# Kernel tuning notes

Hardware: AMD Instinct MI355X
Metric: run time of the kernel (lower is better)

## Reference

```python
import jax, jax.numpy as jnp
import numpy as np

B, T, C, H = 512, 256, 512, 64  # batch, block_size, n_embedding, head_size


def setup_inputs() -> dict:
    key = jax.random.key(0)
    kx, kq, kk, kv = jax.random.split(key, 4)
    # nn.Linear(C, H, bias=False) default init ~ U(-1/sqrt(C), 1/sqrt(C)); stored as x @ W
    s = 1.0 / np.sqrt(C)
    return {
        "x": jax.random.normal(kx, (B, T, C), dtype=jnp.float32),
        "Wq": jax.random.uniform(kq, (C, H), jnp.float32, -s, s),
        "Wk": jax.random.uniform(kk, (C, H), jnp.float32, -s, s),
        "Wv": jax.random.uniform(kv, (C, H), jnp.float32, -s, s),
    }


def reference(x, Wq, Wk, Wv):
    # Projections (bias=False Linear)
    q = x @ Wq  # [B,T,H]
    k = x @ Wk  # [B,T,H]
    v = x @ Wv  # [B,T,H]
    scale = k.shape[-1] ** -0.5
    wei = jnp.einsum('bqh,bkh->bqk', q, k) * scale  # [B,T,T]
    causal = jnp.tril(jnp.ones((x.shape[1], x.shape[1]), dtype=bool))
    wei = jnp.where(causal, wei, -jnp.inf)
    wei = jax.nn.softmax(wei, axis=-1)
    # dropout p=0.0 (eval-mode reference) -> identity
    return wei @ v  # [B,T,H]
```

## Files before the change

kernel.cpp:

```cpp
#include <hip/hip_runtime.h>
#include <hip/hip_bf16.h>

typedef __bf16 bf16;
typedef __bf16 bf16x8 __attribute__((ext_vector_type(8)));
typedef __bf16 bf16x4 __attribute__((ext_vector_type(4)));
typedef float  f32x4  __attribute__((ext_vector_type(4)));

#define MFMA16(a,b,c) __builtin_amdgcn_mfma_f32_16x16x32_bf16((a),(b),(c),0,0,0)

__device__ __forceinline__ void gld16(const void* g, void* l) {
    __builtin_amdgcn_global_load_lds(
        (const __attribute__((address_space(1))) void*)g,
        (__attribute__((address_space(3))) void*)l, 16, 0, 0);
}


__global__ void __launch_bounds__(256) wt_frag_kernel(
        const float* __restrict__ Wq, const float* __restrict__ Wk,
        const float* __restrict__ Wv, bf16* __restrict__ WTfrag) {
    int tid = blockIdx.x * 256 + threadIdx.x;
    int j  = tid & 7;
    int l  = (tid >> 3) & 63;
    int f  = tid >> 9;
    int nf = f % 12;
    int KC = f / 12;
    int k   = KC * 32 + (l >> 4) * 8 + j;
    int col = (nf & 3) * 16 + (l & 15);
    const float* W = (nf < 4) ? Wq : ((nf < 8) ? Wk : Wv);
    WTfrag[tid] = (bf16)W[k * 64 + col];
}

__global__ void __launch_bounds__(256, 1) fused_kernel(
        const float* __restrict__ x, const bf16* __restrict__ WTfrag,
        float* __restrict__ out) {
    extern __shared__ char smem[];

    const int tid = threadIdx.x;
    const int l   = tid & 63;
    const int w   = tid >> 6;
    const int lo  = l & 15;
    const int hi  = l >> 4;
    const int b   = blockIdx.x;
    const char* xb = (const char*)x + (size_t)b * 524288;
    const char* wb = (const char*)WTfrag;

    auto stage = [&](int buf, int kc) {
        #pragma unroll
        for (int j = 0; j < 8; ++j) {
            const int s   = j * 256 + tid;
            const int row = s >> 3;
            const int uP  = s & 7;
            const int uL  = uP ^ (row & 7);
            gld16(xb + (size_t)row * 2048 + kc * 128 + uL * 16,
                  smem + buf * 32768 + s * 16);
        }
        #pragma unroll
        for (int j = 0; j < 3; ++j) {
            const int s = j * 256 + tid;
            gld16(wb + kc * 12288 + s * 16,
                  smem + 65536 + buf * 12288 + s * 16);
        }
    };

    f32x4 acc[4][12];
    #pragma unroll
    for (int mq = 0; mq < 4; ++mq)
        #pragma unroll
        for (int nf = 0; nf < 12; ++nf)
            acc[mq][nf] = (f32x4){0.f, 0.f, 0.f, 0.f};

    auto compute = [&](int buf) {
        bf16x8 a[4];
        #pragma unroll
        for (int mq = 0; mq < 4; ++mq) {
            const int row = w * 64 + mq * 16 + lo;
            const int u0  = (hi * 2)     ^ (lo & 7);
            const int u1  = (hi * 2 + 1) ^ (lo & 7);
            f32x4 v0 = *(const f32x4*)(smem + buf * 32768 + row * 128 + u0 * 16);
            f32x4 v1 = *(const f32x4*)(smem + buf * 32768 + row * 128 + u1 * 16);
            bf16x8 t;
            t[0] = (bf16)v0[0]; t[1] = (bf16)v0[1]; t[2] = (bf16)v0[2]; t[3] = (bf16)v0[3];
            t[4] = (bf16)v1[0]; t[5] = (bf16)v1[1]; t[6] = (bf16)v1[2]; t[7] = (bf16)v1[3];
            a[mq] = t;
        }
        #pragma unroll
        for (int nf = 0; nf < 12; ++nf) {
            bf16x8 bf_ = *(const bf16x8*)(smem + 65536 + buf * 12288 +
                                          nf * 1024 + l * 16);
            #pragma unroll
            for (int mq = 0; mq < 4; ++mq)
                acc[mq][nf] = MFMA16(a[mq], bf_, acc[mq][nf]);
        }
    };

    stage(0, 0);

    #pragma unroll 1
    for (int k = 0; k < 16; ++k) {
        __builtin_amdgcn_s_barrier();
        if (k + 1 < 16) {
            stage((k + 1) & 1, k + 1);
            asm volatile("s_waitcnt vmcnt(11)" ::: "memory");
        } else {
            asm volatile("s_waitcnt vmcnt(0)" ::: "memory");
        }
        __builtin_amdgcn_s_barrier();
        __builtin_amdgcn_sched_barrier(0);
        compute(k & 1);
    }

    __syncthreads();
    {
        char* Qb = smem;
        char* Kb = smem + 32768;
        char* Vb = smem + 65536;
        #pragma unroll
        for (int nf = 0; nf < 12; ++nf) {
            #pragma unroll
            for (int mq = 0; mq < 4; ++mq) {
                #pragma unroll
                for (int i = 0; i < 4; ++i) {
                    bf16 v = (bf16)acc[mq][nf][i];
                    if (nf < 8) {
                        const int row = w * 64 + mq * 16 + hi * 4 + i;
                        const int col = (nf & 3) * 16 + lo;
                        const int u   = col >> 3;
                        char* base = (nf < 4) ? Qb : Kb;
                        *(bf16*)(base + row * 128 + ((u ^ (row & 7)) << 4) +
                                 (col & 7) * 2) = v;
                    } else {
                        const int h = (nf - 8) * 16 + lo;
                        const int t = w * 64 + mq * 16 + hi * 4 + i;
                        const int u = t >> 3;
                        *(bf16*)(Vb + h * 512 + ((u ^ (h & 7)) << 4) +
                                 (t & 7) * 2) = v;
                    }
                }
            }
        }
    }
    __syncthreads();

    const char* Qb = smem;
    const char* Kb = smem + 32768;
    const char* Vb = smem + 65536;
    bf16* Pl = (bf16*)(smem + 98304) + w * (16 * 72);

    bf16x8 qfr[4][2];
    #pragma unroll
    for (int qf = 0; qf < 4; ++qf)
        #pragma unroll
        for (int ks = 0; ks < 2; ++ks) {
            const int q = qf * 64 + w * 16 + lo;
            const int u = ks * 4 + hi;
            qfr[qf][ks] = *(const bf16x8*)(Qb + q * 128 + ((u ^ (lo & 7)) << 4));
        }

    f32x4 o[4][4];
    #pragma unroll
    for (int qf = 0; qf < 4; ++qf)
        #pragma unroll
        for (int mf = 0; mf < 4; ++mf)
            o[qf][mf] = (f32x4){0.f, 0.f, 0.f, 0.f};
    float m2[4]   = {-INFINITY, -INFINITY, -INFINITY, -INFINITY};
    float lsum[4] = {0.f, 0.f, 0.f, 0.f};

    const float SC = 0.125f * 1.44269504088896340736f;

    #pragma unroll
    for (int kc = 0; kc < 4; ++kc) {
        bf16x8 vf[4][2];
        #pragma unroll
        for (int mf = 0; mf < 4; ++mf)
            #pragma unroll
            for (int ks = 0; ks < 2; ++ks) {
                const int h = mf * 16 + lo;
                const int u = kc * 8 + ks * 4 + hi;
                vf[mf][ks] = *(const bf16x8*)(Vb + h * 512 + ((u ^ (lo & 7)) << 4));
            }

        #pragma unroll
        for (int qf = kc; qf < 4; ++qf) {
            f32x4 s[4];
            #pragma unroll
            for (int kf = 0; kf < 4; ++kf) {
                const int key = kc * 64 + kf * 16 + lo;
                bf16x8 k0 = *(const bf16x8*)(Kb + key * 128 + ((hi ^ (lo & 7)) << 4));
                bf16x8 k1 = *(const bf16x8*)(Kb + key * 128 + (((4 + hi) ^ (lo & 7)) << 4));
                f32x4 t = (f32x4){0.f, 0.f, 0.f, 0.f};
                t = MFMA16(k0, qfr[qf][0], t);
                t = MFMA16(k1, qfr[qf][1], t);
                s[kf] = t;
            }
            float mx = -INFINITY;
            #pragma unroll
            for (int kf = 0; kf < 4; ++kf)
                #pragma unroll
                for (int i = 0; i < 4; ++i) {
                    float v = s[kf][i] * SC;
                    if (kc == qf && (kf * 16 + hi * 4 + i) > (w * 16 + lo)) v = -INFINITY;
                    s[kf][i] = v;
                    mx = fmaxf(mx, v);
                }
            mx = fmaxf(mx, __shfl_xor(mx, 16));
            mx = fmaxf(mx, __shfl_xor(mx, 32));
            const float mnew = fmaxf(m2[qf], mx);
            const float rsc  = exp2f(m2[qf] - mnew);
            m2[qf] = mnew;

            float cs = 0.f;
            bf16x4 pk[4];
            #pragma unroll
            for (int kf = 0; kf < 4; ++kf)
                #pragma unroll
                for (int i = 0; i < 4; ++i) {
                    float p = exp2f(s[kf][i] - mnew);
                    cs += p;
                    pk[kf][i] = (bf16)p;
                }
            cs += __shfl_xor(cs, 16);
            cs += __shfl_xor(cs, 32);
            lsum[qf] = lsum[qf] * rsc + cs;

            #pragma unroll
            for (int kf = 0; kf < 4; ++kf)
                *(bf16x4*)(Pl + lo * 72 + kf * 16 + hi * 4) = pk[kf];

            #pragma unroll
            for (int mf = 0; mf < 4; ++mf) {
                o[qf][mf][0] *= rsc; o[qf][mf][1] *= rsc;
                o[qf][mf][2] *= rsc; o[qf][mf][3] *= rsc;
            }
            #pragma unroll
            for (int ks = 0; ks < 2; ++ks) {
                bf16x8 pf = *(const bf16x8*)(Pl + lo * 72 + ks * 32 + hi * 8);
                #pragma unroll
                for (int mf = 0; mf < 4; ++mf)
                    o[qf][mf] = MFMA16(vf[mf][ks], pf, o[qf][mf]);
            }
        }
    }

    #pragma unroll
    for (int qf = 0; qf < 4; ++qf) {
        const float inv = 1.0f / lsum[qf];
        const int q = qf * 64 + w * 16 + lo;
        #pragma unroll
        for (int mf = 0; mf < 4; ++mf) {
            f32x4 r4;
            r4[0] = o[qf][mf][0] * inv; r4[1] = o[qf][mf][1] * inv;
            r4[2] = o[qf][mf][2] * inv; r4[3] = o[qf][mf][3] * inv;
            *(f32x4*)(out + (b * 256 + q) * 64 + mf * 16 + hi * 4) = r4;
        }
    }
}

extern "C" void kernel_launch(void* const* d_in, const int* in_sizes, int n_in,
                              void* d_out, int out_size, void* d_ws, size_t ws_size,
                              hipStream_t stream) {
    const float* x  = (const float*)d_in[0];
    const float* Wq = (const float*)d_in[1];
    const float* Wk = (const float*)d_in[2];
    const float* Wv = (const float*)d_in[3];
    float* out = (float*)d_out;

    bf16* WTfrag = (bf16*)d_ws;

    wt_frag_kernel<<<dim3(384), dim3(256), 0, stream>>>(Wq, Wk, Wv, WTfrag);
    fused_kernel<<<dim3(512), dim3(256), 107520, stream>>>(x, WTfrag, out);
}
```

Measured before the change: 82.69 us.

## Single-buffer projection stage and shrink LDS to fit two blocks per CU

Replaces the double-buffered cp.async-style x/W staging with a single buffer synchronized by __syncthreads, remaps rows so each wave owns strided query rows, and routes Q through a per-wave scratch tile instead of a full Q buffer in LDS. LDS drops from about 105KB to 73KB and launch bounds request two blocks per CU, aiming to overlap blocks rather than overlap loads within a block. The tradeoff is losing intra-block load/compute pipelining and adding barriers, plus register pressure from the 2-occupancy bound with 48 accumulator vectors, which may cause spills.

```diff
diff --git a/kernel.cpp b/kernel.cpp
--- a/kernel.cpp
+++ b/kernel.cpp
@@ -30,7 +30,7 @@
     WTfrag[tid] = (bf16)W[k * 64 + col];
 }
 
-__global__ void __launch_bounds__(256, 1) fused_kernel(
+__global__ void __launch_bounds__(256, 2) fused_kernel(
         const float* __restrict__ x, const bf16* __restrict__ WTfrag,
         float* __restrict__ out) {
     extern __shared__ char smem[];
@@ -44,7 +44,15 @@
     const char* xb = (const char*)x + (size_t)b * 524288;
     const char* wb = (const char*)WTfrag;
 
-    auto stage = [&](int buf, int kc) {
+    f32x4 acc[4][12];
+    #pragma unroll
+    for (int mq = 0; mq < 4; ++mq)
+        #pragma unroll
+        for (int nf = 0; nf < 12; ++nf)
+            acc[mq][nf] = (f32x4){0.f, 0.f, 0.f, 0.f};
+
+    #pragma unroll 1
+    for (int kc = 0; kc < 16; ++kc) {
         #pragma unroll
         for (int j = 0; j < 8; ++j) {
             const int s   = j * 256 + tid;
@@ -52,32 +60,23 @@
             const int uP  = s & 7;
             const int uL  = uP ^ (row & 7);
             gld16(xb + (size_t)row * 2048 + kc * 128 + uL * 16,
-                  smem + buf * 32768 + s * 16);
+                  smem + s * 16);
         }
         #pragma unroll
         for (int j = 0; j < 3; ++j) {
             const int s = j * 256 + tid;
-            gld16(wb + kc * 12288 + s * 16,
-                  smem + 65536 + buf * 12288 + s * 16);
-        }
-    };
-
-    f32x4 acc[4][12];
-    #pragma unroll
-    for (int mq = 0; mq < 4; ++mq)
-        #pragma unroll
-        for (int nf = 0; nf < 12; ++nf)
-            acc[mq][nf] = (f32x4){0.f, 0.f, 0.f, 0.f};
-
-    auto compute = [&](int buf) {
+            gld16(wb + kc * 12288 + s * 16, smem + 32768 + s * 16);
+        }
+        __syncthreads();
+
         bf16x8 a[4];
         #pragma unroll
         for (int mq = 0; mq < 4; ++mq) {
-            const int row = w * 64 + mq * 16 + lo;
+            const int row = mq * 64 + w * 16 + lo;
             const int u0  = (hi * 2)     ^ (lo & 7);
             const int u1  = (hi * 2 + 1) ^ (lo & 7);
-            f32x4 v0 = *(const f32x4*)(smem + buf * 32768 + row * 128 + u0 * 16);
-            f32x4 v1 = *(const f32x4*)(smem + buf * 32768 + row * 128 + u1 * 16);
+            f32x4 v0 = *(const f32x4*)(smem + row * 128 + u0 * 16);
+            f32x4 v1 = *(const f32x4*)(smem + row * 128 + u1 * 16);
             bf16x8 t;
             t[0] = (bf16)v0[0]; t[1] = (bf16)v0[1]; t[2] = (bf16)v0[2]; t[3] = (bf16)v0[3];
             t[4] = (bf16)v1[0]; t[5] = (bf16)v1[1]; t[6] = (bf16)v1[2]; t[7] = (bf16)v1[3];
@@ -85,76 +84,55 @@
         }
         #pragma unroll
         for (int nf = 0; nf < 12; ++nf) {
-            bf16x8 bf_ = *(const bf16x8*)(smem + 65536 + buf * 12288 +
-                                          nf * 1024 + l * 16);
+            bf16x8 bf_ = *(const bf16x8*)(smem + 32768 + nf * 1024 + l * 16);
             #pragma unroll
             for (int mq = 0; mq < 4; ++mq)
                 acc[mq][nf] = MFMA16(a[mq], bf_, acc[mq][nf]);
         }
-    };
-
-    stage(0, 0);
-
-    #pragma unroll 1
-    for (int k = 0; k < 16; ++k) {
-        __builtin_amdgcn_s_barrier();
-        if (k + 1 < 16) {
-            stage((k + 1) & 1, k + 1);
-            asm volatile("s_waitcnt vmcnt(11)" ::: "memory");
-        } else {
-            asm volatile("s_waitcnt vmcnt(0)" ::: "memory");
-        }
-        __builtin_amdgcn_s_barrier();
-        __builtin_amdgcn_sched_barrier(0);
-        compute(k & 1);
-    }
-
-    __syncthreads();
-    {
-        char* Qb = smem;
-        char* Kb = smem + 32768;
-        char* Vb = smem + 65536;
-        #pragma unroll
-        for (int nf = 0; nf < 12; ++nf) {
-            #pragma unroll
-            for (int mq = 0; mq < 4; ++mq) {
-                #pragma unroll
-                for (int i = 0; i < 4; ++i) {
-                    bf16 v = (bf16)acc[mq][nf][i];
-                    if (nf < 8) {
-                        const int row = w * 64 + mq * 16 + hi * 4 + i;
-                        const int col = (nf & 3) * 16 + lo;
-                        const int u   = col >> 3;
-                        char* base = (nf < 4) ? Qb : Kb;
-                        *(bf16*)(base + row * 128 + ((u ^ (row & 7)) << 4) +
-                                 (col & 7) * 2) = v;
-                    } else {
-                        const int h = (nf - 8) * 16 + lo;
-                        const int t = w * 64 + mq * 16 + hi * 4 + i;
-                        const int u = t >> 3;
-                        *(bf16*)(Vb + h * 512 + ((u ^ (h & 7)) << 4) +
-                                 (t & 7) * 2) = v;
-                    }
+        __syncthreads();
+    }
+
+    char* Kb = smem;
+    char* Vb = smem + 32768;
+    #pragma unroll
+    for (int nf = 4; nf < 12; ++nf) {
+        #pragma unroll
+        for (int mq = 0; mq < 4; ++mq) {
+            #pragma unroll
+            for (int i = 0; i < 4; ++i) {
+                bf16 v = (bf16)acc[mq][nf][i];
+                if (nf < 8) {
+                    const int row = mq * 64 + w * 16 + hi * 4 + i;
+                    const int col = (nf - 4) * 16 + lo;
+                    const int u   = col >> 3;
+                    *(bf16*)(Kb + row * 128 + ((u ^ (row & 7)) << 4) +
+                             (col & 7) * 2) = v;
+                } else {
+                    const int h = (nf - 8) * 16 + lo;
+                    const int t = mq * 64 + w * 16 + hi * 4 + i;
+                    const int u = t >> 3;
+                    *(bf16*)(Vb + h * 512 + ((u ^ (h & 7)) << 4) +
+                             (t & 7) * 2) = v;
                 }
             }
         }
     }
-    __syncthreads();
-
-    const char* Qb = smem;
-    const char* Kb = smem + 32768;
-    const char* Vb = smem + 65536;
-    bf16* Pl = (bf16*)(smem + 98304) + w * (16 * 72);
-
+
+    bf16* Pl = (bf16*)(smem + 65536) + w * 1152;
     bf16x8 qfr[4][2];
     #pragma unroll
-    for (int qf = 0; qf < 4; ++qf)
-        #pragma unroll
-        for (int ks = 0; ks < 2; ++ks) {
-            const int q = qf * 64 + w * 16 + lo;
-            const int u = ks * 4 + hi;
-            qfr[qf][ks] = *(const bf16x8*)(Qb + q * 128 + ((u ^ (lo & 7)) << 4));
-        }
+    for (int qf = 0; qf < 4; ++qf) {
+        #pragma unroll
+        for (int nf = 0; nf < 4; ++nf)
+            #pragma unroll
+            for (int i = 0; i < 4; ++i)
+                Pl[(hi * 4 + i) * 72 + nf * 16 + lo] = (bf16)acc[qf][nf][i];
+        __syncthreads();
+        #pragma unroll
+        for (int ks = 0; ks < 2; ++ks)
+            qfr[qf][ks] = *(const bf16x8*)(Pl + lo * 72 + ks * 32 + hi * 8);
+        __syncthreads();
+    }
 
     f32x4 o[4][4];
     #pragma unroll
@@ -267,5 +245,5 @@
     bf16* WTfrag = (bf16*)d_ws;
 
     wt_frag_kernel<<<dim3(384), dim3(256), 0, stream>>>(Wq, Wk, Wv, WTfrag);
-    fused_kernel<<<dim3(512), dim3(256), 107520, stream>>>(x, WTfrag, out);
-}
+    fused_kernel<<<dim3(512), dim3(256), 74752, stream>>>(x, WTfrag, out);
+}
```

Result: faster. 71.81 us (-13.2%).
